# Kernel optimization log

Measured on AMD Instinct MI355X. Metric: run time of the kernel, lower is better.

The kernel has to match this reference:

```python
import jax, jax.numpy as jnp
import numpy as np

B, IN_DIM, K, D = 8192, 1024, 2048, 256
TAU = 1.0
BN_EPS = 1e-5


def setup_inputs() -> dict:
    key = jax.random.key(0)
    ks = jax.random.split(key, 4)
    x = jax.random.normal(ks[0], (B, IN_DIM), dtype=jnp.float32)
    u = jax.random.uniform(ks[1], (B, K), dtype=jnp.float32)  # uniform for gumbel noise
    W = jax.random.normal(ks[2], (IN_DIM, D), dtype=jnp.float32) * 0.02
    b = jnp.zeros((D,), dtype=jnp.float32)
    gamma = jnp.ones((D,), dtype=jnp.float32)
    beta = jnp.zeros((D,), dtype=jnp.float32)
    E = jax.random.normal(ks[3], (K, D), dtype=jnp.float32)  # nn.Embedding default N(0,1)
    return {"x": x, "u": u, "W": W, "b": b, "gamma": gamma, "beta": beta, "E": E}


def reference(x, u, W, b, gamma, beta, E):
    # classifier + BatchNorm1d (training mode: batch stats, biased variance)
    h = x @ W + b                                   # [B, D]
    mu = jnp.mean(h, axis=0)
    var = jnp.var(h, axis=0)
    h = (h - mu) * jax.lax.rsqrt(var + BN_EPS) * gamma + beta
    # negative squared euclidean distance via ||h||^2 - 2 h.E^T + ||e||^2 (GEMM form,
    # avoids materializing [B, K, D])
    h2 = jnp.sum(h * h, axis=-1, keepdims=True)     # [B, 1]
    e2 = jnp.sum(E * E, axis=-1)                    # [K]
    logits = -(h2 - 2.0 * (h @ E.T) + e2)           # [B, K]
    # gumbel-softmax (soft) with tau
    g = -jnp.log(-jnp.log(u + 1e-10) + 1e-10)
    assignments = jax.nn.softmax((logits + g) / TAU, axis=-1)  # [B, K]
    z = assignments @ E                             # [B, D]
    probs = jax.nn.softmax(logits, axis=-1)
    return probs, z
```

## Files before the change

### kernel.cpp

```cpp
#include <hip/hip_runtime.h>
#include <math.h>

#define B_SZ 8192
#define IN_DIM 1024
#define K_CB 2048
#define D_SZ 256
#define BN_EPS 1e-5f

typedef _Float16 f16;
typedef _Float16 f16x8 __attribute__((ext_vector_type(8)));
typedef _Float16 f16x4 __attribute__((ext_vector_type(4)));
typedef float    f32x4 __attribute__((ext_vector_type(4)));

#define GLOAD_LDS16(g, l) __builtin_amdgcn_global_load_lds(                      \
    (const __attribute__((address_space(1))) unsigned int*)(g),                  \
    (__attribute__((address_space(3))) unsigned int*)(l), 16, 0, 0)

template<int BM, int BN, int BK, int EPI, bool A32>
__global__ __launch_bounds__(256) void gemm_mfma(
    const void* __restrict__ Aptr, int lda,
    const f16* __restrict__ Bptr, int ldb,
    void* __restrict__ Cptr, int ldc, int Kdim,
    const float* __restrict__ bias)
{
    constexpr int G    = BK / 8;
    constexpr int MASK = G - 1;
    constexpr int WM = BM / 2, WN = BN / 2;
    constexpr int FM = WM / 16, FN = WN / 16;
    constexpr int CH_A = BM * G;
    constexpr int CH_B = BN * G;

    __shared__ char lds[(BM + BN) * BK * 2];
    char* As = lds;
    char* Bs = lds + BM * BK * 2;

    const int tid  = threadIdx.x;
    const int w    = tid >> 6, lane = tid & 63;
    const int wm   = w >> 1,   wn   = w & 1;
    const int row0 = blockIdx.x * BM;
    const int col0 = blockIdx.y * BN;

    f32x4 acc[FM][FN] = {};

    for (int k0 = 0; k0 < Kdim; k0 += BK) {
        #pragma unroll
        for (int i = 0; i < CH_B / 256; ++i) {
            const int base = (i * 4 + w) * 64;
            const int s = base + lane;
            const int r = s / G, c = s % G;
            const f16* src = Bptr + (size_t)(col0 + r) * ldb + k0 + ((c ^ (r & MASK)) * 8);
            GLOAD_LDS16(src, Bs + base * 16);
        }
        if (!A32) {
            #pragma unroll
            for (int i = 0; i < CH_A / 256; ++i) {
                const int base = (i * 4 + w) * 64;
                const int s = base + lane;
                const int r = s / G, c = s % G;
                const f16* src = (const f16*)Aptr + (size_t)(row0 + r) * lda + k0 + ((c ^ (r & MASK)) * 8);
                GLOAD_LDS16(src, As + base * 16);
            }
        } else {
            #pragma unroll
            for (int i = 0; i < CH_A / 256; ++i) {
                const int s = i * 256 + tid;
                const int r = s / G, c = s % G;
                const float* src = (const float*)Aptr + (size_t)(row0 + r) * lda + k0 + c * 8;
                const float4 v0 = ((const float4*)src)[0];
                const float4 v1 = ((const float4*)src)[1];
                f16x8 d;
                d[0] = (f16)v0.x; d[1] = (f16)v0.y; d[2] = (f16)v0.z; d[3] = (f16)v0.w;
                d[4] = (f16)v1.x; d[5] = (f16)v1.y; d[6] = (f16)v1.z; d[7] = (f16)v1.w;
                *(f16x8*)(As + (r * G + (c ^ (r & MASK))) * 16) = d;
            }
        }
        __syncthreads();

        #pragma unroll
        for (int kk = 0; kk < BK / 32; ++kk) {
            f16x8 af[FM], bf[FN];
            #pragma unroll
            for (int m = 0; m < FM; ++m) {
                const int r = wm * WM + m * 16 + (lane & 15);
                const int g = (kk * 4 + (lane >> 4)) ^ (r & MASK);
                af[m] = *(const f16x8*)(As + r * (BK * 2) + g * 16);
            }
            #pragma unroll
            for (int n = 0; n < FN; ++n) {
                const int r = wn * WN + n * 16 + (lane & 15);
                const int g = (kk * 4 + (lane >> 4)) ^ (r & MASK);
                bf[n] = *(const f16x8*)(Bs + r * (BK * 2) + g * 16);
            }
            #pragma unroll
            for (int m = 0; m < FM; ++m)
                #pragma unroll
                for (int n = 0; n < FN; ++n)
                    acc[m][n] = __builtin_amdgcn_mfma_f32_16x16x32_f16(af[m], bf[n], acc[m][n], 0, 0, 0);
        }
        __syncthreads();
    }

    #pragma unroll
    for (int m = 0; m < FM; ++m) {
        const int rbase = row0 + wm * WM + m * 16 + (lane >> 4) * 4;
        #pragma unroll
        for (int n = 0; n < FN; ++n) {
            const int c = col0 + wn * WN + n * 16 + (lane & 15);
            #pragma unroll
            for (int j = 0; j < 4; ++j) {
                const float v = acc[m][n][j];
                if (EPI == 0) {
                    ((float*)Cptr)[(size_t)(rbase + j) * ldc + c] = v;
                } else {
                    ((f16*)Cptr)[(size_t)(rbase + j) * ldc + c] = (f16)(v + bias[c]);
                }
            }
        }
    }
}

#define LP1 2056

__global__ __launch_bounds__(1024, 1) void fused_sm(
    const f16* __restrict__ h16, const f16* __restrict__ E16,
    const float* __restrict__ e2v, const float* __restrict__ u,
    const float* __restrict__ scale, const float* __restrict__ shift,
    float* __restrict__ probs, f16* __restrict__ assign16)
{
    __shared__ __align__(16) char lds_raw[32 * LP1 * 2];
    __shared__ float redA[16 * 16];
    f16* Bs0 = (f16*)lds_raw;
    f16* Bs1 = Bs0 + 128 * 256;
    f16* p1buf = (f16*)lds_raw;

    const int tid  = threadIdx.x;
    const int w    = tid >> 6, lane = tid & 63;
    const int q    = lane >> 4, r16 = lane & 15;
    const int g2   = w >> 3;
    const int wc   = w & 7;
    const int row0 = blockIdx.x * 32;
    const int rowA = row0 + g2 * 16;
    const int colL = wc * 16 + r16;

    f16x8 af[8];
    {
        const f16* hrow = h16 + (size_t)(rowA + r16) * D_SZ + q * 8;
        #pragma unroll
        for (int kk = 0; kk < 8; ++kk) {
            const f16x8 raw = *(const f16x8*)(hrow + kk * 32);
            const float4 scA = *(const float4*)(scale + kk * 32 + q * 8);
            const float4 scB = *(const float4*)(scale + kk * 32 + q * 8 + 4);
            const float4 shA = *(const float4*)(shift + kk * 32 + q * 8);
            const float4 shB = *(const float4*)(shift + kk * 32 + q * 8 + 4);
            f16x8 d;
            d[0] = (f16)fmaf((float)raw[0], scA.x, shA.x);
            d[1] = (f16)fmaf((float)raw[1], scA.y, shA.y);
            d[2] = (f16)fmaf((float)raw[2], scA.z, shA.z);
            d[3] = (f16)fmaf((float)raw[3], scA.w, shA.w);
            d[4] = (f16)fmaf((float)raw[4], scB.x, shB.x);
            d[5] = (f16)fmaf((float)raw[5], scB.y, shB.y);
            d[6] = (f16)fmaf((float)raw[6], scB.z, shB.z);
            d[7] = (f16)fmaf((float)raw[7], scB.w, shB.w);
            af[kk] = d;
        }
    }

    f32x4 acc[16];
    #pragma unroll
    for (int n = 0; n < 16; ++n) acc[n] = (f32x4){0.f, 0.f, 0.f, 0.f};

    #pragma unroll
    for (int i = 0; i < 4; ++i) {
        const int base = (i * 16 + w) * 64;
        const int s = base + lane;
        const int r = s >> 5, cgg = s & 31;
        GLOAD_LDS16(E16 + (size_t)r * D_SZ + ((cgg ^ (r & 31)) * 8), Bs0 + base * 8);
    }

    #pragma unroll
    for (int c = 0; c < 16; ++c) {
        f16* buf  = (c & 1) ? Bs1 : Bs0;
        f16* nbuf = (c & 1) ? Bs0 : Bs1;
        if (c < 15) {
            #pragma unroll
            for (int i = 0; i < 4; ++i) {
                const int base = (i * 16 + w) * 64;
                const int s = base + lane;
                const int r = s >> 5, cgg = s & 31;
                GLOAD_LDS16(E16 + (size_t)((c + 1) * 128 + r) * D_SZ + ((cgg ^ (r & 31)) * 8),
                            nbuf + base * 8);
            }
            asm volatile("s_waitcnt vmcnt(4)" ::: "memory");
        } else {
            asm volatile("s_waitcnt vmcnt(0)" ::: "memory");
        }
        __builtin_amdgcn_s_barrier();
        __builtin_amdgcn_sched_barrier(0);
        #pragma unroll
        for (int kk = 0; kk < 8; ++kk) {
            const int gb = (kk * 4 + q) ^ (colL & 31);
            const f16x8 bf = *(const f16x8*)(buf + colL * 256 + gb * 8);
            acc[c] = __builtin_amdgcn_mfma_f32_16x16x32_f16(af[kk], bf, acc[c], 0, 0, 0);
        }
        __builtin_amdgcn_sched_barrier(0);
        __builtin_amdgcn_s_barrier();
        __builtin_amdgcn_sched_barrier(0);
    }
    __syncthreads();

    float m1[4] = {-1e30f, -1e30f, -1e30f, -1e30f};
    #pragma unroll
    for (int n = 0; n < 16; ++n) {
        const float ec = e2v[n * 128 + colL];
        #pragma unroll
        for (int j = 0; j < 4; ++j)
            m1[j] = fmaxf(m1[j], 2.f * acc[n][j] - ec);
    }
    #pragma unroll
    for (int off = 1; off < 16; off <<= 1)
        #pragma unroll
        for (int j = 0; j < 4; ++j)
            m1[j] = fmaxf(m1[j], __shfl_xor(m1[j], off));
    if (r16 == 0)
        #pragma unroll
        for (int j = 0; j < 4; ++j) redA[w * 16 + q * 4 + j] = m1[j];
    __syncthreads();
    #pragma unroll
    for (int j = 0; j < 4; ++j) {
        float a = -1e30f;
        #pragma unroll
        for (int t = 0; t < 8; ++t) a = fmaxf(a, redA[(g2 * 8 + t) * 16 + q * 4 + j]);
        m1[j] = a;
    }

    #pragma unroll
    for (int n = 0; n < 16; ++n) {
        const float ec = e2v[n * 128 + colL];
        #pragma unroll
        for (int j = 0; j < 4; ++j) {
            const float lv = 2.f * acc[n][j] - ec;
            p1buf[(size_t)(g2 * 16 + q * 4 + j) * LP1 + n * 128 + colL] =
                (f16)__expf(lv - m1[j] + 10.f);
        }
    }
    __syncthreads();

    const int trow = tid >> 5;
    const int cg   = tid & 31;
    const float* urow = u + (size_t)(row0 + trow) * K_CB + cg * 4;
    const f16* prow_l = p1buf + (size_t)trow * LP1 + cg * 4;

    float s1 = 0.f, s2 = 0.f;
    f16x4 p1f[16];
    f32x4 t[16];
    #pragma unroll
    for (int n = 0; n < 16; ++n) {
        const float4 u4 = *(const float4*)(urow + n * 128);
        const f16x4 p4 = *(const f16x4*)(prow_l + n * 128);
        const float ua[4] = {u4.x, u4.y, u4.z, u4.w};
        p1f[n] = p4;
        #pragma unroll
        for (int e = 0; e < 4; ++e) {
            const float g = -__logf(-__logf(ua[e] + 1e-10f) + 1e-10f);
            const float te = (float)p4[e] * __expf(g);
            t[n][e] = te;
            s1 += (float)p4[e];
            s2 += te;
        }
    }
    #pragma unroll
    for (int off = 1; off < 32; off <<= 1) {
        s1 += __shfl_xor(s1, off);
        s2 += __shfl_xor(s2, off);
    }
    const float r1 = 1.f / s1;
    const float r2 = 1.f / s2;

    float* prow = probs + (size_t)(row0 + trow) * K_CB + cg * 4;
    f16* arow = assign16 + (size_t)(row0 + trow) * K_CB + cg * 4;
    #pragma unroll
    for (int n = 0; n < 16; ++n) {
        float4 o;
        o.x = (float)p1f[n][0] * r1; o.y = (float)p1f[n][1] * r1;
        o.z = (float)p1f[n][2] * r1; o.w = (float)p1f[n][3] * r1;
        *(float4*)(prow + n * 128) = o;
        f16x4 a4;
        #pragma unroll
        for (int e = 0; e < 4; ++e) a4[e] = (f16)(t[n][e] * r2);
        *(f16x4*)(arow + n * 128) = a4;
    }
}

__global__ __launch_bounds__(256) void conv_WT(const float* __restrict__ W, f16* __restrict__ WT)
{
    const int r = blockIdx.x, c = threadIdx.x;
    WT[c * 1024 + r] = (f16)W[r * 256 + c];
}

__global__ __launch_bounds__(256) void conv_E2(const float* __restrict__ E,
                                               f16* __restrict__ E16, f16* __restrict__ ET,
                                               float* __restrict__ e2)
{
    const int r = blockIdx.x, c = threadIdx.x;
    const int wave = c >> 6, lane = c & 63;
    const float v = E[r * 256 + c];
    E16[r * 256 + c] = (f16)v;
    ET[c * 2048 + r] = (f16)v;
    float ss = v * v;
    #pragma unroll
    for (int off = 32; off > 0; off >>= 1) ss += __shfl_down(ss, off);
    __shared__ float s4[4];
    if (lane == 0) s4[wave] = ss;
    __syncthreads();
    if (c == 0) e2[r] = s4[0] + s4[1] + s4[2] + s4[3];
}

__global__ __launch_bounds__(256) void bn_partial(const f16* __restrict__ h16, float* __restrict__ part)
{
    const int d = threadIdx.x;
    const int blk = blockIdx.x;
    const int r0 = blk * (B_SZ / 128);
    float s = 0.f, sq = 0.f;
    for (int r = r0; r < r0 + (B_SZ / 128); ++r) {
        const float v = (float)h16[(size_t)r * D_SZ + d];
        s += v; sq += v * v;
    }
    part[blk * 512 + d]       = s;
    part[blk * 512 + 256 + d] = sq;
}

__global__ __launch_bounds__(256) void bn_finalize(
    const float* __restrict__ part, const float* __restrict__ gamma, const float* __restrict__ beta,
    float* __restrict__ scale, float* __restrict__ shift)
{
    const int d = threadIdx.x;
    float s = 0.f, sq = 0.f;
    for (int b = 0; b < 128; ++b) { s += part[b * 512 + d]; sq += part[b * 512 + 256 + d]; }
    const float mu  = s / (float)B_SZ;
    const float var = sq / (float)B_SZ - mu * mu;
    const float sc  = gamma[d] * rsqrtf(var + BN_EPS);
    scale[d] = sc;
    shift[d] = beta[d] - mu * sc;
}

extern "C" void kernel_launch(void* const* d_in, const int* in_sizes, int n_in,
                              void* d_out, int out_size, void* d_ws, size_t ws_size,
                              hipStream_t stream)
{
    const float* x     = (const float*)d_in[0];
    const float* u     = (const float*)d_in[1];
    const float* W     = (const float*)d_in[2];
    const float* bias  = (const float*)d_in[3];
    const float* gamma = (const float*)d_in[4];
    const float* beta  = (const float*)d_in[5];
    const float* E     = (const float*)d_in[6];

    float* probs = (float*)d_out;
    float* z     = probs + (size_t)B_SZ * K_CB;

    char* ws = (char*)d_ws;
    f16* assign16 = (f16*)ws;  ws += (size_t)B_SZ * K_CB * 2;
    f16* h16 = (f16*)ws;       ws += (size_t)B_SZ * D_SZ * 2;
    f16* WT16 = (f16*)ws;      ws += (size_t)D_SZ * IN_DIM * 2;
    f16* E16 = (f16*)ws;       ws += (size_t)K_CB * D_SZ * 2;
    f16* ET16 = (f16*)ws;      ws += (size_t)D_SZ * K_CB * 2;
    float* part = (float*)ws;  ws += 128 * 512 * 4;
    float* scale = (float*)ws; ws += D_SZ * 4;
    float* shift = (float*)ws; ws += D_SZ * 4;
    float* e2 = (float*)ws;    ws += K_CB * 4;

    conv_WT<<<IN_DIM, 256, 0, stream>>>(W, WT16);
    conv_E2<<<K_CB, 256, 0, stream>>>(E, E16, ET16, e2);

    {
        dim3 g(B_SZ / 64, D_SZ / 64);
        gemm_mfma<64, 64, 64, 1, true><<<g, 256, 0, stream>>>(
            x, IN_DIM, WT16, IN_DIM, h16, D_SZ, IN_DIM, bias);
    }
    bn_partial<<<128, 256, 0, stream>>>(h16, part);
    bn_finalize<<<1, 256, 0, stream>>>(part, gamma, beta, scale, shift);

    fused_sm<<<B_SZ / 32, 1024, 0, stream>>>(h16, E16, e2, u, scale, shift, probs, assign16);

    {
        dim3 g(B_SZ / 64, D_SZ / 64);
        gemm_mfma<64, 64, 128, 0, false><<<g, 256, 0, stream>>>(
            assign16, K_CB, ET16, K_CB, z, D_SZ, K_CB, nullptr);
    }
}
```

Baseline: 120.9 us.

## Fuse assignments@E GEMM into softmax kernel, keeping assignments in LDS

The final z = assignments @ E GEMM moves into the fused softmax kernel. Assignments are written back into the LDS p1 buffer instead of a global fp16 workspace, and each block then runs MFMAs against ET16 read directly from global memory. This removes the global write and re-read of the B×K fp16 assignment matrix and one kernel launch. Gumbel noise is kept as fp16 to cut register pressure, and waves_per_eu is pinned. The costs are redundant per-block reads of ET16 without LDS staging, an extra fp16 rounding of the noise, and a longer kernel.

```diff
diff --git a/kernel.cpp b/kernel.cpp
--- a/kernel.cpp
+++ b/kernel.cpp
@@ -121,11 +121,13 @@
 
 #define LP1 2056
 
-__global__ __launch_bounds__(1024, 1) void fused_sm(
+__global__ __attribute__((amdgpu_waves_per_eu(4, 4))) __launch_bounds__(1024)
+void fused_sm(
     const f16* __restrict__ h16, const f16* __restrict__ E16,
-    const float* __restrict__ e2v, const float* __restrict__ u,
-    const float* __restrict__ scale, const float* __restrict__ shift,
-    float* __restrict__ probs, f16* __restrict__ assign16)
+    const f16* __restrict__ ET16, const float* __restrict__ e2v,
+    const float* __restrict__ u, const float* __restrict__ scale,
+    const float* __restrict__ shift,
+    float* __restrict__ probs, float* __restrict__ z)
 {
     __shared__ __align__(16) char lds_raw[32 * LP1 * 2];
     __shared__ float redA[16 * 16];
@@ -232,7 +234,6 @@
         for (int t = 0; t < 8; ++t) a = fmaxf(a, redA[(g2 * 8 + t) * 16 + q * 4 + j]);
         m1[j] = a;
     }
-
     #pragma unroll
     for (int n = 0; n < 16; ++n) {
         const float ec = e2v[n * 128 + colL];
@@ -248,24 +249,21 @@
     const int trow = tid >> 5;
     const int cg   = tid & 31;
     const float* urow = u + (size_t)(row0 + trow) * K_CB + cg * 4;
-    const f16* prow_l = p1buf + (size_t)trow * LP1 + cg * 4;
+    f16* prow_l = p1buf + (size_t)trow * LP1 + cg * 4;
 
     float s1 = 0.f, s2 = 0.f;
-    f16x4 p1f[16];
-    f32x4 t[16];
+    f16x4 gv[16];
     #pragma unroll
     for (int n = 0; n < 16; ++n) {
         const float4 u4 = *(const float4*)(urow + n * 128);
         const f16x4 p4 = *(const f16x4*)(prow_l + n * 128);
         const float ua[4] = {u4.x, u4.y, u4.z, u4.w};
-        p1f[n] = p4;
         #pragma unroll
         for (int e = 0; e < 4; ++e) {
-            const float g = -__logf(-__logf(ua[e] + 1e-10f) + 1e-10f);
-            const float te = (float)p4[e] * __expf(g);
-            t[n][e] = te;
+            const f16 g = (f16)(-__logf(-__logf(ua[e] + 1e-10f) + 1e-10f));
+            gv[n][e] = g;
             s1 += (float)p4[e];
-            s2 += te;
+            s2 += (float)p4[e] * __expf((float)g);
         }
     }
     #pragma unroll
@@ -277,17 +275,40 @@
     const float r2 = 1.f / s2;
 
     float* prow = probs + (size_t)(row0 + trow) * K_CB + cg * 4;
-    f16* arow = assign16 + (size_t)(row0 + trow) * K_CB + cg * 4;
     #pragma unroll
     for (int n = 0; n < 16; ++n) {
+        const f16x4 p4 = *(const f16x4*)(prow_l + n * 128);
         float4 o;
-        o.x = (float)p1f[n][0] * r1; o.y = (float)p1f[n][1] * r1;
-        o.z = (float)p1f[n][2] * r1; o.w = (float)p1f[n][3] * r1;
+        o.x = (float)p4[0] * r1; o.y = (float)p4[1] * r1;
+        o.z = (float)p4[2] * r1; o.w = (float)p4[3] * r1;
         *(float4*)(prow + n * 128) = o;
         f16x4 a4;
         #pragma unroll
-        for (int e = 0; e < 4; ++e) a4[e] = (f16)(t[n][e] * r2);
-        *(f16x4*)(arow + n * 128) = a4;
+        for (int e = 0; e < 4; ++e)
+            a4[e] = (f16)((float)p4[e] * __expf((float)gv[n][e]) * r2);
+        *(f16x4*)(prow_l + n * 128) = a4;
+    }
+    __syncthreads();
+
+    f32x4 acc2[2] = {};
+    const f16* p2row = p1buf + (size_t)(g2 * 16 + r16) * LP1 + q * 8;
+    const f16* et0 = ET16 + (size_t)(wc * 32 + r16) * K_CB + q * 8;
+    const f16* et1 = ET16 + (size_t)(wc * 32 + 16 + r16) * K_CB + q * 8;
+    #pragma unroll
+    for (int ks = 0; ks < 64; ++ks) {
+        const f16x8 a8 = *(const f16x8*)(p2row + ks * 32);
+        const f16x8 b0 = *(const f16x8*)(et0 + ks * 32);
+        const f16x8 b1 = *(const f16x8*)(et1 + ks * 32);
+        acc2[0] = __builtin_amdgcn_mfma_f32_16x16x32_f16(a8, b0, acc2[0], 0, 0, 0);
+        acc2[1] = __builtin_amdgcn_mfma_f32_16x16x32_f16(a8, b1, acc2[1], 0, 0, 0);
+    }
+    #pragma unroll
+    for (int t2 = 0; t2 < 2; ++t2) {
+        const int col = wc * 32 + t2 * 16 + r16;
+        #pragma unroll
+        for (int j = 0; j < 4; ++j) {
+            z[(size_t)(rowA + q * 4 + j) * D_SZ + col] = acc2[t2][j];
+        }
     }
 }
 
@@ -359,7 +380,6 @@
     float* z     = probs + (size_t)B_SZ * K_CB;
 
     char* ws = (char*)d_ws;
-    f16* assign16 = (f16*)ws;  ws += (size_t)B_SZ * K_CB * 2;
     f16* h16 = (f16*)ws;       ws += (size_t)B_SZ * D_SZ * 2;
     f16* WT16 = (f16*)ws;      ws += (size_t)D_SZ * IN_DIM * 2;
     f16* E16 = (f16*)ws;       ws += (size_t)K_CB * D_SZ * 2;
@@ -380,11 +400,6 @@
     bn_partial<<<128, 256, 0, stream>>>(h16, part);
     bn_finalize<<<1, 256, 0, stream>>>(part, gamma, beta, scale, shift);
 
-    fused_sm<<<B_SZ / 32, 1024, 0, stream>>>(h16, E16, e2, u, scale, shift, probs, assign16);
-
-    {
-        dim3 g(B_SZ / 64, D_SZ / 64);
-        gemm_mfma<64, 64, 128, 0, false><<<g, 256, 0, stream>>>(
-            assign16, K_CB, ET16, K_CB, z, D_SZ, K_CB, nullptr);
-    }
-}
+    fused_sm<<<B_SZ / 32, 1024, 0, stream>>>(h16, E16, ET16, e2, u,
+                                             scale, shift, probs, z);
+}
```

Result: slower. 152.1 us (+25.8%).
